# Optimization experiments

Measured on AMD Instinct MI355X. Metric: run time of the kernel, lower is better.

Reference implementation:

```python
import jax, jax.numpy as jnp
import numpy as np

# Blade metric for Cl(1,3) inner product <~A B>_0: sign per basis blade =
# (-1)^{k(k-1)/2} * prod(eta_ii) with eta = diag(1,-1,-1,-1).
# Order: 1 | e0 e1 e2 e3 | e01 e02 e03 e12 e13 e23 | e012 e013 e023 e123 | e0123
BLADE_METRIC = jnp.array(
    [1.0,
     1.0, -1.0, -1.0, -1.0,
     1.0, 1.0, 1.0, -1.0, -1.0, -1.0,
     -1.0, -1.0, -1.0, 1.0,
     -1.0],
    dtype=jnp.float32,
)

B, H, N, MVC, SC = 8, 8, 1024, 8, 32


def setup_inputs() -> dict:
    key = jax.random.key(0)
    ks = jax.random.split(key, 6)
    mv_shape = (B, H, N, MVC, 16)
    s_shape = (B, H, N, SC)
    return {
        "q_mv": jax.random.normal(ks[0], mv_shape, dtype=jnp.float32),
        "k_mv": jax.random.normal(ks[1], mv_shape, dtype=jnp.float32),
        "v_mv": jax.random.normal(ks[2], mv_shape, dtype=jnp.float32),
        "q_s": jax.random.normal(ks[3], s_shape, dtype=jnp.float32),
        "k_s": jax.random.normal(ks[4], s_shape, dtype=jnp.float32),
        "v_s": jax.random.normal(ks[5], s_shape, dtype=jnp.float32),
    }


def reference(q_mv, k_mv, v_mv, q_s, k_s, v_s):
    *lead, n_out, mvc, _ = q_mv.shape
    n_in = k_mv.shape[-3]
    sc = q_s.shape[-1]
    d = 16 * mvc + sc  # total feature dim used for the softmax scale

    # Apply GA blade metric to queries, flatten mv channels, concat scalars.
    qf = jnp.concatenate(
        [(q_mv * BLADE_METRIC).reshape(*lead, n_out, mvc * 16), q_s], axis=-1
    )
    kf = jnp.concatenate([k_mv.reshape(*lead, n_in, mvc * 16), k_s], axis=-1)
    vf = jnp.concatenate([v_mv.reshape(*lead, n_in, mvc * 16), v_s], axis=-1)

    scores = jnp.einsum("bhid,bhjd->bhij", qf, kf) / jnp.sqrt(
        jnp.asarray(d, dtype=qf.dtype)
    )
    attn = jax.nn.softmax(scores, axis=-1)
    out = jnp.einsum("bhij,bhjd->bhid", attn, vf)

    out_mv = out[..., : mvc * 16].reshape(*lead, n_out, mvc, 16)
    out_s = out[..., mvc * 16 :]
    return out_mv, out_s
```

## Files before the change

### kernel.cpp

```cpp
#include <hip/hip_runtime.h>

typedef __attribute__((ext_vector_type(8))) _Float16 f16x8;
typedef __attribute__((ext_vector_type(4))) float f32x4;

#define BHn 64
#define Nn 1024

static constexpr int kOutMvElems = 8 * 8 * 1024 * 128;
static constexpr float kScaleLog2e = 0.11405506f;
static constexpr unsigned kNegMask = 0xBF1Cu;
static constexpr int kBlob = 20480;
static constexpr int kPair = 2 * kBlob;

typedef __attribute__((address_space(1))) const void* gas1_t;
typedef __attribute__((address_space(3))) void* las3_t;
__device__ __forceinline__ void dma16(const _Float16* g, _Float16* l) {
  __builtin_amdgcn_global_load_lds((gas1_t)g, (las3_t)l, 16, 0, 0);
}
__device__ __forceinline__ float fast_exp2(float x) {
  float r;
  asm("v_exp_f32 %0, %1" : "=v"(r) : "v"(x));
  return r;
}

__global__ __launch_bounds__(256) void pack_kernel(const float* __restrict__ kmv,
                                                   const float* __restrict__ ks,
                                                   const float* __restrict__ vmv,
                                                   const float* __restrict__ vs,
                                                   _Float16* __restrict__ KV) {
  __shared__ _Float16 tk[64][184];
  __shared__ _Float16 tv[160][72];
  const int kt = blockIdx.x;
  const int bh = blockIdx.y;
  const int tid = threadIdx.x;
#pragma unroll
  for (int i = 0; i < 5; ++i) {
    int s = tid + 256 * i;
    int key = s / 20, p = s - key * 20;
    int row = bh * Nn + kt * 64 + key;
    const float* src = (p < 16) ? (kmv + (size_t)row * 128 + p * 8)
                                : (ks + (size_t)row * 32 + (p - 16) * 8);
    float4 a = *(const float4*)src;
    float4 b = *(const float4*)(src + 4);
    f16x8 h;
    h[0] = (_Float16)a.x; h[1] = (_Float16)a.y; h[2] = (_Float16)a.z; h[3] = (_Float16)a.w;
    h[4] = (_Float16)b.x; h[5] = (_Float16)b.y; h[6] = (_Float16)b.z; h[7] = (_Float16)b.w;
    *(f16x8*)&tk[key][p * 8] = h;
  }
  for (int s = tid; s < 64 * 40; s += 256) {
    int key = s / 40, p = s - key * 40;
    int row = bh * Nn + kt * 64 + key;
    const float* src = (p < 32) ? (vmv + (size_t)row * 128 + p * 4)
                                : (vs + (size_t)row * 32 + (p - 32) * 4);
    float4 v = *(const float4*)src;
    int d = p * 4;
    tv[d + 0][key] = (_Float16)v.x;
    tv[d + 1][key] = (_Float16)v.y;
    tv[d + 2][key] = (_Float16)v.z;
    tv[d + 3][key] = (_Float16)v.w;
  }
  __syncthreads();
  _Float16* dst = KV + ((size_t)bh * 16 + kt) * kBlob;
#pragma unroll
  for (int i = 0; i < 5; ++i) {
    int u = tid + 256 * i;
    int p = u >> 6, key = u & 63;
    f16x8 h = *(const f16x8*)&tk[key][p * 8];
    *(f16x8*)&dst[p * 512 + key * 8] = h;
  }
#pragma unroll
  for (int i = 0; i < 5; ++i) {
    int u = tid + 256 * i;
    int s = u / 160, d = u - s * 160;
    int c32 = (s >> 2) * 32, gg = s & 3;
    f16x8 h;
#pragma unroll
    for (int i2 = 0; i2 < 8; ++i2) {
      int key = c32 + ((i2 < 4) ? (gg * 4 + i2) : (16 + gg * 4 + (i2 - 4)));
      h[i2] = tv[d][key];
    }
    *(f16x8*)&dst[10240 + u * 8] = h;
  }
}

__global__ __launch_bounds__(512, 1) void geo_attn_kernel(const float* __restrict__ qmv,
                                                          const float* __restrict__ qs,
                                                          const _Float16* __restrict__ KV,
                                                          float* __restrict__ out) {
  __shared__ __align__(16) _Float16 kv[2 * kPair];

  const int b = blockIdx.x;
  const int sw = (b & 7) * 32 + (b >> 3);
  const int qb = sw & 3;
  const int bh = sw >> 2;

  const int tid = threadIdx.x;
  const int w = tid >> 6;
  const int l = tid & 63;
  const int g = l >> 4;
  const int nn = l & 15;

  const _Float16* blob0 = KV + (size_t)bh * 16 * kBlob;

  int kbase[5];
#pragma unroll
  for (int c = 0; c < 5; ++c) kbase[c] = (4 * c + g) * 512 + nn * 8;
  int vbase[2];
#pragma unroll
  for (int ch = 0; ch < 2; ++ch) vbase[ch] = 10240 + (4 * ch + g) * 1280 + nn * 8;

  f16x8 qf[2][5];
#pragma unroll
  for (int q2 = 0; q2 < 2; ++q2) {
    const size_t qbase = (size_t)(bh * Nn + qb * 256 + w * 32 + q2 * 16 + nn);
#pragma unroll
    for (int c = 0; c < 5; ++c) {
      const float* src = (c < 4) ? (qmv + qbase * 128 + c * 32 + 8 * g)
                                 : (qs + qbase * 32 + 8 * g);
      float4 a = *(const float4*)src;
      float4 bb = *(const float4*)(src + 4);
      float x[8] = {a.x, a.y, a.z, a.w, bb.x, bb.y, bb.z, bb.w};
#pragma unroll
      for (int i = 0; i < 8; ++i) {
        float v = x[i] * kScaleLog2e;
        if (c < 4) {
          int idx = ((g & 1) << 3) + i;
          v = ((kNegMask >> idx) & 1u) ? -v : v;
        }
        qf[q2][c][i] = (_Float16)v;
      }
    }
  }

  f32x4 acc[2][10];
#pragma unroll
  for (int q2 = 0; q2 < 2; ++q2)
#pragma unroll
    for (int j = 0; j < 10; ++j) acc[q2][j] = (f32x4){0.f, 0.f, 0.f, 0.f};
  float Ma = 12.f, Mb = 12.f, La = 0.f, Lb = 0.f;

  f32x4 sa[4], sb[4];
  f16x8 paf[2], pbf[2];

  const int laneOff = l * 8 + w * 512;
  auto stage = [&](int t, int buf) {
    const _Float16* src = blob0 + (size_t)t * kPair + laneOff;
    _Float16* dst = &kv[buf * kPair + laneOff];
#pragma unroll
    for (int i = 0; i < 10; ++i) dma16(src + i * 4096, dst + i * 4096);
  };

  auto cluster = [&](const _Float16* kblob, const _Float16* vblob, bool doPV) {
#pragma unroll
    for (int kb = 0; kb < 4; ++kb) {
      sa[kb] = (f32x4){0.f, 0.f, 0.f, 0.f};
      sb[kb] = (f32x4){0.f, 0.f, 0.f, 0.f};
    }
    f16x8 kf[5][4];
    f16x8 vf[20];
#pragma unroll
    for (int kb = 0; kb < 4; ++kb) kf[0][kb] = *(const f16x8*)&kblob[kbase[0] + kb * 128];
    if (doPV) {
#pragma unroll
      for (int i = 0; i < 4; ++i)
        vf[i] = *(const f16x8*)&vblob[vbase[i / 10] + (i % 10) * 128];
    }
#pragma unroll
    for (int c = 0; c < 5; ++c) {
      if (c + 1 < 5) {
#pragma unroll
        for (int kb = 0; kb < 4; ++kb)
          kf[c + 1][kb] = *(const f16x8*)&kblob[kbase[c + 1] + kb * 128];
      }
#pragma unroll
      for (int kb = 0; kb < 4; ++kb) {
        const int i = c * 4 + kb;
        sa[kb] = __builtin_amdgcn_mfma_f32_16x16x32_f16(kf[c][kb], qf[0][c], sa[kb], 0, 0, 0);
        if (doPV && i + 4 < 20)
          vf[i + 4] = *(const f16x8*)&vblob[vbase[(i + 4) / 10] + ((i + 4) % 10) * 128];
        sb[kb] = __builtin_amdgcn_mfma_f32_16x16x32_f16(kf[c][kb], qf[1][c], sb[kb], 0, 0, 0);
        if (doPV) {
          const int ch = i / 10, j = i % 10;
          acc[0][j] = __builtin_amdgcn_mfma_f32_16x16x32_f16(paf[ch], vf[i], acc[0][j], 0, 0, 0);
          acc[1][j] = __builtin_amdgcn_mfma_f32_16x16x32_f16(pbf[ch], vf[i], acc[1][j], 0, 0, 0);
        }
      }
    }
  };
  auto pv_only = [&](const _Float16* vblob) {
    f16x8 vf[4];
#pragma unroll
    for (int i = 0; i < 4; ++i)
      vf[i & 3] = *(const f16x8*)&vblob[vbase[i / 10] + (i % 10) * 128];
#pragma unroll
    for (int i = 0; i < 20; ++i) {
      f16x8 cu = vf[i & 3];
      if (i + 4 < 20)
        vf[i & 3] = *(const f16x8*)&vblob[vbase[(i + 4) / 10] + ((i + 4) % 10) * 128];
      const int ch = i / 10, j = i % 10;
      acc[0][j] = __builtin_amdgcn_mfma_f32_16x16x32_f16(paf[ch], cu, acc[0][j], 0, 0, 0);
      acc[1][j] = __builtin_amdgcn_mfma_f32_16x16x32_f16(pbf[ch], cu, acc[1][j], 0, 0, 0);
    }
  };
  auto do_softmax = [&]() {
    float rsa = 0.f, rsb = 0.f;
#pragma unroll
    for (int kb = 0; kb < 4; ++kb) {
      const int ch = kb >> 1, off = (kb & 1) * 4;
#pragma unroll
      for (int r = 0; r < 4; ++r) {
        float pa_ = fast_exp2(sa[kb][r] - Ma);
        float pb_ = fast_exp2(sb[kb][r] - Mb);
        rsa += pa_; rsb += pb_;
        paf[ch][off + r] = (_Float16)pa_;
        pbf[ch][off + r] = (_Float16)pb_;
      }
    }
    if (__builtin_expect(__any((int)(rsa > 3.2e4f || rsb > 3.2e4f)), 0)) {
      float lma = sa[0][0], lmb = sb[0][0];
#pragma unroll
      for (int kb = 0; kb < 4; ++kb)
#pragma unroll
        for (int r = 0; r < 4; ++r) {
          lma = fmaxf(lma, sa[kb][r]);
          lmb = fmaxf(lmb, sb[kb][r]);
        }
      lma = fmaxf(lma, __shfl_xor(lma, 16)); lma = fmaxf(lma, __shfl_xor(lma, 32));
      lmb = fmaxf(lmb, __shfl_xor(lmb, 16)); lmb = fmaxf(lmb, __shfl_xor(lmb, 32));
      float nMa = fmaxf(Ma, lma); float fsa = fast_exp2(Ma - nMa); Ma = nMa;
      float nMb = fmaxf(Mb, lmb); float fsb = fast_exp2(Mb - nMb); Mb = nMb;
      La *= fsa; Lb *= fsb;
      float fa[4], fb[4];
#pragma unroll
      for (int r = 0; r < 4; ++r) {
        fa[r] = __shfl(fsa, 4 * g + r, 16);
        fb[r] = __shfl(fsb, 4 * g + r, 16);
      }
#pragma unroll
      for (int j = 0; j < 10; ++j)
#pragma unroll
        for (int r = 0; r < 4; ++r) {
          acc[0][j][r] *= fa[r];
          acc[1][j][r] *= fb[r];
        }
      rsa = 0.f; rsb = 0.f;
#pragma unroll
      for (int kb = 0; kb < 4; ++kb) {
        const int ch = kb >> 1, off = (kb & 1) * 4;
#pragma unroll
        for (int r = 0; r < 4; ++r) {
          float pa_ = fast_exp2(sa[kb][r] - Ma);
          float pb_ = fast_exp2(sb[kb][r] - Mb);
          rsa += pa_; rsb += pb_;
          paf[ch][off + r] = (_Float16)pa_;
          pbf[ch][off + r] = (_Float16)pb_;
        }
      }
    }
    La += rsa;
    Lb += rsb;
  };

  stage(0, 0);
  __syncthreads();

  __builtin_amdgcn_s_setprio(1);
  cluster(&kv[0], &kv[0], false);
  __builtin_amdgcn_s_setprio(0);
  do_softmax();
  __syncthreads();
  stage(1, 1);
  __builtin_amdgcn_s_setprio(1);
  cluster(&kv[kBlob], &kv[0], true);
  __builtin_amdgcn_s_setprio(0);
  do_softmax();
  __syncthreads();

  for (int t = 1; t < 8; ++t) {
    const int c = t & 1;
    __builtin_amdgcn_s_setprio(1);
    cluster(&kv[c * kPair], &kv[(c ^ 1) * kPair + kBlob], true);
    __builtin_amdgcn_s_setprio(0);
    do_softmax();
    __syncthreads();
    if (t < 7) stage(t + 1, c ^ 1);
    __builtin_amdgcn_s_setprio(1);
    cluster(&kv[c * kPair + kBlob], &kv[c * kPair], true);
    __builtin_amdgcn_s_setprio(0);
    do_softmax();
    __syncthreads();
  }
  pv_only(&kv[kPair + kBlob]);

  La += __shfl_xor(La, 16); La += __shfl_xor(La, 32);
  Lb += __shfl_xor(Lb, 16); Lb += __shfl_xor(Lb, 32);
  float ria = 1.f / La, rib = 1.f / Lb;
  float ra[4], rb_[4];
#pragma unroll
  for (int r = 0; r < 4; ++r) {
    ra[r] = __shfl(ria, 4 * g + r, 16);
    rb_[r] = __shfl(rib, 4 * g + r, 16);
  }
  const int row0 = bh * Nn + qb * 256 + w * 32;
#pragma unroll
  for (int j = 0; j < 10; ++j) {
    const int d = 16 * j + nn;
#pragma unroll
    for (int r = 0; r < 4; ++r) {
      float v0 = acc[0][j][r] * ra[r];
      float v1 = acc[1][j][r] * rb_[r];
      const int r0 = row0 + 4 * g + r;
      const int r1 = row0 + 16 + 4 * g + r;
      if (d < 128) {
        out[(size_t)r0 * 128 + d] = v0;
        out[(size_t)r1 * 128 + d] = v1;
      } else {
        out[(size_t)kOutMvElems + (size_t)r0 * 32 + (d - 128)] = v0;
        out[(size_t)kOutMvElems + (size_t)r1 * 32 + (d - 128)] = v1;
      }
    }
  }
}

extern "C" void kernel_launch(void* const* d_in, const int* in_sizes, int n_in,
                              void* d_out, int out_size, void* d_ws, size_t ws_size,
                              hipStream_t stream) {
  const float* qmv = (const float*)d_in[0];
  const float* kmv = (const float*)d_in[1];
  const float* vmv = (const float*)d_in[2];
  const float* qs = (const float*)d_in[3];
  const float* ks = (const float*)d_in[4];
  const float* vs = (const float*)d_in[5];
  float* out = (float*)d_out;

  _Float16* KV = (_Float16*)d_ws;

  pack_kernel<<<dim3(16, BHn), dim3(256), 0, stream>>>(kmv, ks, vmv, vs, KV);
  geo_attn_kernel<<<dim3(256), dim3(512), 0, stream>>>(qmv, qs, KV, out);
}
```

Measured before the change: 78.75 us.

## Interleave softmax exp with PV MFMAs using double-buffered probability registers

Restructures the per-tile schedule. The QK MFMAs now run first, and a fused phase issues the previous tile's PV MFMAs while computing the current tile's exp2/softmax values between them. Probabilities are ping-ponged between even and odd register sets so old P can feed the MFMAs while new P is written. The goal is to hide VALU exp work behind matrix-core work. The K fragment prefetch depth also goes from one to two chunks, which adds register pressure that could hurt occupancy.

```diff
diff --git a/kernel.cpp b/kernel.cpp
--- a/kernel.cpp
+++ b/kernel.cpp
@@ -140,7 +140,8 @@
   float Ma = 12.f, Mb = 12.f, La = 0.f, Lb = 0.f;
 
   f32x4 sa[4], sb[4];
-  f16x8 paf[2], pbf[2];
+  f16x8 pafE[2], pbfE[2];
+  f16x8 pafO[2], pbfO[2];
 
   const int laneOff = l * 8 + w * 512;
   auto stage = [&](int t, int buf) {
@@ -150,147 +151,171 @@
     for (int i = 0; i < 10; ++i) dma16(src + i * 4096, dst + i * 4096);
   };
 
-  auto cluster = [&](const _Float16* kblob, const _Float16* vblob, bool doPV) {
+  auto do_qk = [&](const _Float16* blob) {
 #pragma unroll
     for (int kb = 0; kb < 4; ++kb) {
       sa[kb] = (f32x4){0.f, 0.f, 0.f, 0.f};
       sb[kb] = (f32x4){0.f, 0.f, 0.f, 0.f};
     }
     f16x8 kf[5][4];
-    f16x8 vf[20];
-#pragma unroll
-    for (int kb = 0; kb < 4; ++kb) kf[0][kb] = *(const f16x8*)&kblob[kbase[0] + kb * 128];
-    if (doPV) {
-#pragma unroll
-      for (int i = 0; i < 4; ++i)
-        vf[i] = *(const f16x8*)&vblob[vbase[i / 10] + (i % 10) * 128];
-    }
+#pragma unroll
+    for (int c = 0; c < 2; ++c)
+#pragma unroll
+      for (int kb = 0; kb < 4; ++kb) kf[c][kb] = *(const f16x8*)&blob[kbase[c] + kb * 128];
 #pragma unroll
     for (int c = 0; c < 5; ++c) {
-      if (c + 1 < 5) {
+      if (c + 2 < 5) {
 #pragma unroll
         for (int kb = 0; kb < 4; ++kb)
-          kf[c + 1][kb] = *(const f16x8*)&kblob[kbase[c + 1] + kb * 128];
+          kf[c + 2][kb] = *(const f16x8*)&blob[kbase[c + 2] + kb * 128];
       }
 #pragma unroll
       for (int kb = 0; kb < 4; ++kb) {
-        const int i = c * 4 + kb;
         sa[kb] = __builtin_amdgcn_mfma_f32_16x16x32_f16(kf[c][kb], qf[0][c], sa[kb], 0, 0, 0);
-        if (doPV && i + 4 < 20)
-          vf[i + 4] = *(const f16x8*)&vblob[vbase[(i + 4) / 10] + ((i + 4) % 10) * 128];
         sb[kb] = __builtin_amdgcn_mfma_f32_16x16x32_f16(kf[c][kb], qf[1][c], sb[kb], 0, 0, 0);
-        if (doPV) {
-          const int ch = i / 10, j = i % 10;
-          acc[0][j] = __builtin_amdgcn_mfma_f32_16x16x32_f16(paf[ch], vf[i], acc[0][j], 0, 0, 0);
-          acc[1][j] = __builtin_amdgcn_mfma_f32_16x16x32_f16(pbf[ch], vf[i], acc[1][j], 0, 0, 0);
-        }
-      }
-    }
-  };
-  auto pv_only = [&](const _Float16* vblob) {
+      }
+    }
+  };
+
+  auto sm_slow = [&](f16x8 (&pN)[2], f16x8 (&qN)[2], float& rsa, float& rsb) {
+    float lma = sa[0][0], lmb = sb[0][0];
+#pragma unroll
+    for (int kb = 0; kb < 4; ++kb)
+#pragma unroll
+      for (int r = 0; r < 4; ++r) {
+        lma = fmaxf(lma, sa[kb][r]);
+        lmb = fmaxf(lmb, sb[kb][r]);
+      }
+    lma = fmaxf(lma, __shfl_xor(lma, 16)); lma = fmaxf(lma, __shfl_xor(lma, 32));
+    lmb = fmaxf(lmb, __shfl_xor(lmb, 16)); lmb = fmaxf(lmb, __shfl_xor(lmb, 32));
+    float nMa = fmaxf(Ma, lma); float fsa = fast_exp2(Ma - nMa); Ma = nMa;
+    float nMb = fmaxf(Mb, lmb); float fsb = fast_exp2(Mb - nMb); Mb = nMb;
+    La *= fsa; Lb *= fsb;
+    float fa[4], fb[4];
+#pragma unroll
+    for (int r = 0; r < 4; ++r) {
+      fa[r] = __shfl(fsa, 4 * g + r, 16);
+      fb[r] = __shfl(fsb, 4 * g + r, 16);
+    }
+#pragma unroll
+    for (int j = 0; j < 10; ++j)
+#pragma unroll
+      for (int r = 0; r < 4; ++r) {
+        acc[0][j][r] *= fa[r];
+        acc[1][j][r] *= fb[r];
+      }
+    rsa = 0.f; rsb = 0.f;
+#pragma unroll
+    for (int kb = 0; kb < 4; ++kb) {
+      const int ch = kb >> 1, off = (kb & 1) * 4;
+#pragma unroll
+      for (int r = 0; r < 4; ++r) {
+        float pa_ = fast_exp2(sa[kb][r] - Ma);
+        float pb_ = fast_exp2(sb[kb][r] - Mb);
+        rsa += pa_; rsb += pb_;
+        pN[ch][off + r] = (_Float16)pa_;
+        qN[ch][off + r] = (_Float16)pb_;
+      }
+    }
+  };
+
+  auto do_softmax = [&](f16x8 (&pN)[2], f16x8 (&qN)[2]) {
+    float rsa = 0.f, rsb = 0.f;
+#pragma unroll
+    for (int kb = 0; kb < 4; ++kb) {
+      const int ch = kb >> 1, off = (kb & 1) * 4;
+#pragma unroll
+      for (int r = 0; r < 4; ++r) {
+        float pa_ = fast_exp2(sa[kb][r] - Ma);
+        float pb_ = fast_exp2(sb[kb][r] - Mb);
+        rsa += pa_; rsb += pb_;
+        pN[ch][off + r] = (_Float16)pa_;
+        qN[ch][off + r] = (_Float16)pb_;
+      }
+    }
+    if (__builtin_expect(__any((int)(rsa > 3.2e4f || rsb > 3.2e4f)), 0))
+      sm_slow(pN, qN, rsa, rsb);
+    La += rsa;
+    Lb += rsb;
+  };
+
+  auto fused = [&](const _Float16* vblob, f16x8 (&pOld)[2], f16x8 (&qOld)[2],
+                   f16x8 (&pNew)[2], f16x8 (&qNew)[2]) {
+    float rsa = 0.f, rsb = 0.f;
     f16x8 vf[4];
 #pragma unroll
     for (int i = 0; i < 4; ++i)
-      vf[i & 3] = *(const f16x8*)&vblob[vbase[i / 10] + (i % 10) * 128];
+      vf[i] = *(const f16x8*)&vblob[vbase[i / 10] + (i % 10) * 128];
 #pragma unroll
     for (int i = 0; i < 20; ++i) {
       f16x8 cu = vf[i & 3];
       if (i + 4 < 20)
         vf[i & 3] = *(const f16x8*)&vblob[vbase[(i + 4) / 10] + ((i + 4) % 10) * 128];
       const int ch = i / 10, j = i % 10;
-      acc[0][j] = __builtin_amdgcn_mfma_f32_16x16x32_f16(paf[ch], cu, acc[0][j], 0, 0, 0);
-      acc[1][j] = __builtin_amdgcn_mfma_f32_16x16x32_f16(pbf[ch], cu, acc[1][j], 0, 0, 0);
-    }
-  };
-  auto do_softmax = [&]() {
-    float rsa = 0.f, rsb = 0.f;
-#pragma unroll
-    for (int kb = 0; kb < 4; ++kb) {
-      const int ch = kb >> 1, off = (kb & 1) * 4;
-#pragma unroll
-      for (int r = 0; r < 4; ++r) {
+      acc[0][j] = __builtin_amdgcn_mfma_f32_16x16x32_f16(pOld[ch], cu, acc[0][j], 0, 0, 0);
+      if (i < 16) {
+        const int kb = i >> 2, r = i & 3;
+        const int ch2 = kb >> 1, off = (kb & 1) * 4;
         float pa_ = fast_exp2(sa[kb][r] - Ma);
         float pb_ = fast_exp2(sb[kb][r] - Mb);
         rsa += pa_; rsb += pb_;
-        paf[ch][off + r] = (_Float16)pa_;
-        pbf[ch][off + r] = (_Float16)pb_;
-      }
-    }
-    if (__builtin_expect(__any((int)(rsa > 3.2e4f || rsb > 3.2e4f)), 0)) {
-      float lma = sa[0][0], lmb = sb[0][0];
-#pragma unroll
-      for (int kb = 0; kb < 4; ++kb)
-#pragma unroll
-        for (int r = 0; r < 4; ++r) {
-          lma = fmaxf(lma, sa[kb][r]);
-          lmb = fmaxf(lmb, sb[kb][r]);
-        }
-      lma = fmaxf(lma, __shfl_xor(lma, 16)); lma = fmaxf(lma, __shfl_xor(lma, 32));
-      lmb = fmaxf(lmb, __shfl_xor(lmb, 16)); lmb = fmaxf(lmb, __shfl_xor(lmb, 32));
-      float nMa = fmaxf(Ma, lma); float fsa = fast_exp2(Ma - nMa); Ma = nMa;
-      float nMb = fmaxf(Mb, lmb); float fsb = fast_exp2(Mb - nMb); Mb = nMb;
-      La *= fsa; Lb *= fsb;
-      float fa[4], fb[4];
-#pragma unroll
-      for (int r = 0; r < 4; ++r) {
-        fa[r] = __shfl(fsa, 4 * g + r, 16);
-        fb[r] = __shfl(fsb, 4 * g + r, 16);
-      }
-#pragma unroll
-      for (int j = 0; j < 10; ++j)
-#pragma unroll
-        for (int r = 0; r < 4; ++r) {
-          acc[0][j][r] *= fa[r];
-          acc[1][j][r] *= fb[r];
-        }
-      rsa = 0.f; rsb = 0.f;
-#pragma unroll
-      for (int kb = 0; kb < 4; ++kb) {
-        const int ch = kb >> 1, off = (kb & 1) * 4;
-#pragma unroll
-        for (int r = 0; r < 4; ++r) {
-          float pa_ = fast_exp2(sa[kb][r] - Ma);
-          float pb_ = fast_exp2(sb[kb][r] - Mb);
-          rsa += pa_; rsb += pb_;
-          paf[ch][off + r] = (_Float16)pa_;
-          pbf[ch][off + r] = (_Float16)pb_;
-        }
-      }
-    }
+        pNew[ch2][off + r] = (_Float16)pa_;
+        qNew[ch2][off + r] = (_Float16)pb_;
+      }
+      acc[1][j] = __builtin_amdgcn_mfma_f32_16x16x32_f16(qOld[ch], cu, acc[1][j], 0, 0, 0);
+    }
+    if (__builtin_expect(__any((int)(rsa > 3.2e4f || rsb > 3.2e4f)), 0))
+      sm_slow(pNew, qNew, rsa, rsb);
     La += rsa;
     Lb += rsb;
   };
 
+  auto pv_only = [&](const _Float16* vblob, f16x8 (&pOld)[2], f16x8 (&qOld)[2]) {
+    f16x8 vf[4];
+#pragma unroll
+    for (int i = 0; i < 4; ++i)
+      vf[i] = *(const f16x8*)&vblob[vbase[i / 10] + (i % 10) * 128];
+#pragma unroll
+    for (int i = 0; i < 20; ++i) {
+      f16x8 cu = vf[i & 3];
+      if (i + 4 < 20)
+        vf[i & 3] = *(const f16x8*)&vblob[vbase[(i + 4) / 10] + ((i + 4) % 10) * 128];
+      const int ch = i / 10, j = i % 10;
+      acc[0][j] = __builtin_amdgcn_mfma_f32_16x16x32_f16(pOld[ch], cu, acc[0][j], 0, 0, 0);
+      acc[1][j] = __builtin_amdgcn_mfma_f32_16x16x32_f16(qOld[ch], cu, acc[1][j], 0, 0, 0);
+    }
+  };
+
   stage(0, 0);
   __syncthreads();
 
   __builtin_amdgcn_s_setprio(1);
-  cluster(&kv[0], &kv[0], false);
+  do_qk(&kv[0]);
   __builtin_amdgcn_s_setprio(0);
-  do_softmax();
+  do_softmax(pafE, pbfE);
   __syncthreads();
   stage(1, 1);
   __builtin_amdgcn_s_setprio(1);
-  cluster(&kv[kBlob], &kv[0], true);
+  do_qk(&kv[kBlob]);
+  fused(&kv[0], pafE, pbfE, pafO, pbfO);
   __builtin_amdgcn_s_setprio(0);
-  do_softmax();
   __syncthreads();
 
   for (int t = 1; t < 8; ++t) {
     const int c = t & 1;
     __builtin_amdgcn_s_setprio(1);
-    cluster(&kv[c * kPair], &kv[(c ^ 1) * kPair + kBlob], true);
+    do_qk(&kv[c * kPair]);
+    fused(&kv[(c ^ 1) * kPair + kBlob], pafO, pbfO, pafE, pbfE);
     __builtin_amdgcn_s_setprio(0);
-    do_softmax();
     __syncthreads();
     if (t < 7) stage(t + 1, c ^ 1);
     __builtin_amdgcn_s_setprio(1);
-    cluster(&kv[c * kPair + kBlob], &kv[c * kPair], true);
+    do_qk(&kv[c * kPair + kBlob]);
+    fused(&kv[c * kPair], pafE, pbfE, pafO, pbfO);
     __builtin_amdgcn_s_setprio(0);
-    do_softmax();
     __syncthreads();
   }
-  pv_only(&kv[kPair + kBlob]);
+  pv_only(&kv[kPair + kBlob], pafO, pbfO);
 
   La += __shfl_xor(La, 16); La += __shfl_xor(La, 32);
   Lb += __shfl_xor(Lb, 16); Lb += __shfl_xor(Lb, 32);
```

Result: no change. 78.84 us (+0.1%).
